# Performance work log

Hardware: AMD Instinct MI355X
Metric: run time of the kernel (lower is better)

## Reference

```python
import jax, jax.numpy as jnp
import numpy as np

GAMMA = 0.99  # init kwarg


def _discounted_returns(ep_rs):
    # reversed running_add = running_add*gamma + r, emitted per step
    def step(carry, r):
        carry = carry * GAMMA + r
        return carry, carry
    _, out = jax.lax.scan(step, jnp.float32(0.0), ep_rs, reverse=True)
    return out  # [T]


def setup_inputs() -> dict:
    key = jax.random.key(0)
    k1, k2, k3 = jax.random.split(key, 3)
    T, A = 2097152, 18
    weight = jax.random.normal(k1, (T, A), dtype=jnp.float32)
    ep_rs = jax.random.normal(k2, (T,), dtype=jnp.float32)
    ep_as = jax.random.randint(k3, (T,), 0, A, dtype=jnp.int64)
    return {"weight": weight, "ep_rs": ep_rs, "ep_as": ep_as}


def reference(weight, ep_rs, ep_as):
    d = _discounted_returns(ep_rs)
    d = d - jnp.mean(d)
    # cross_entropy with reduction='none': -log_softmax(weight)[t, ep_as[t]]
    logp = jax.nn.log_softmax(weight, axis=-1)  # [T, A]
    neg_log_prob = -jnp.take_along_axis(logp, ep_as[:, None], axis=-1)[:, 0]  # [T]
    return jnp.mean(neg_log_prob * d)
```

## Files before the change

### kernel.cpp

```cpp
#include <hip/hip_runtime.h>
#include <math.h>

#define T_TOTAL 2097152
#define A_DIM   18
#define GAMMA_D 0.99

#define CHUNK 256
#define NC    (T_TOTAL / CHUNK)
#define KTR   14
#define CPB   2
#define NB    (NC / CPB)
#define BLK   256
#define WIN   (CPB + KTR - 1)

constexpr double Gp1   = GAMMA_D;
constexpr double Gp2   = Gp1 * Gp1;
constexpr double Gp4   = Gp2 * Gp2;
constexpr double Gp8   = Gp4 * Gp4;
constexpr double Gp16  = Gp8 * Gp8;
constexpr double Gp32  = Gp16 * Gp16;
constexpr double Gp64  = Gp32 * Gp32;
constexpr double Gp128 = Gp64 * Gp64;
constexpr double Gp256 = Gp128 * Gp128;
constexpr double IG    = 1.0 / GAMMA_D;

__global__ __launch_bounds__(BLK, 6)
void k_mega(const float* __restrict__ wgt, const int* __restrict__ act,
            const float* __restrict__ r, double* __restrict__ partials) {
    __shared__ double ldsL[WIN];
    __shared__ double ldsD[CPB * CHUNK];
    __shared__ double red[12];
    const int tid  = threadIdx.x;
    const int lane = tid & 63, wv = tid >> 6;
    const int c0   = blockIdx.x * CPB;
    const double g = GAMMA_D;
    double w4 = 1.0;
    w4 *= (lane & 1)  ? Gp4   : 1.0;
    w4 *= (lane & 2)  ? Gp8   : 1.0;
    w4 *= (lane & 4)  ? Gp16  : 1.0;
    w4 *= (lane & 8)  ? Gp32  : 1.0;
    w4 *= (lane & 16) ? Gp64  : 1.0;
    w4 *= (lane & 32) ? Gp128 : 1.0;

    float4 rwin[4];
    #pragma unroll
    for (int i = 0; i < 4; ++i) {
        const int k  = wv + 4 * i;
        const int cc = c0 + 1 + k;
        rwin[i] = (k < WIN && cc < NC)
                  ? ((const float4*)r)[(size_t)cc * 64 + lane]
                  : make_float4(0, 0, 0, 0);
    }
    const float4 rown = (wv < CPB)
                        ? ((const float4*)r)[(size_t)(c0 + wv) * 64 + lane]
                        : make_float4(0, 0, 0, 0);

    #pragma unroll
    for (int i = 0; i < 4; ++i) {
        const int k = wv + 4 * i;
        if (k < WIN) {
            double val = w4 * ((double)rwin[i].x + g * ((double)rwin[i].y +
                         g * ((double)rwin[i].z + g * (double)rwin[i].w)));
            #pragma unroll
            for (int off = 32; off > 0; off >>= 1) val += __shfl_down(val, off, 64);
            if (lane == 0) ldsL[k] = val;
        }
    }
    __syncthreads();

    if (wv < CPB) {
        double acc_c = 0.0, wG = 1.0;
        #pragma unroll
        for (int m = 0; m < KTR; ++m) { acc_c += wG * ldsL[wv + m]; wG *= Gp256; }
        const double u3 = (double)rown.w;
        const double u2 = (double)rown.z + g * u3;
        const double u1 = (double)rown.y + g * u2;
        const double u0 = (double)rown.x + g * u1;
        double S = w4 * u0;
        #pragma unroll
        for (int off = 1; off < 64; off <<= 1) {
            const double t = __shfl_down(S, off, 64);
            S += (lane + off < 64) ? t : 0.0;
        }
        double Snext = __shfl_down(S, 1, 64);
        if (lane == 63) Snext = 0.0;
        const double A = (1.0 / w4) * (Snext + Gp256 * acc_c);
        double* dp = ldsD + wv * CHUNK + 4 * lane;
        dp[0] = u0 + A;
        dp[1] = u1 + IG * A;
        dp[2] = u2 + (IG * IG) * A;
        dp[3] = u3 + (IG * IG * IG) * A;
    }
    __syncthreads();

    const size_t t0 = (size_t)blockIdx.x * (CPB * CHUNK) + 2 * (size_t)tid;
    float w[36];
    float4* aw = (float4*)w;
    const float4* wp = (const float4*)(wgt + t0 * A_DIM);
    #pragma unroll
    for (int q = 0; q < 9; ++q) aw[q] = wp[q];
    const int2    aa = *(const int2*)(act + t0);
    const double2 dd = *(const double2*)(ldsD + 2 * tid);

    double s_n = 0.0, s_nd = 0.0;
    double s_d = dd.x + dd.y;
    {
        float mx = w[0];
        #pragma unroll
        for (int j = 1; j < A_DIM; ++j) mx = fmaxf(mx, w[j]);
        float s = 0.0f, wsel = 0.0f;
        #pragma unroll
        for (int j = 0; j < A_DIM; ++j) { s += __expf(w[j] - mx); wsel = (j == aa.x) ? w[j] : wsel; }
        const float nlp = mx + __logf(s) - wsel;
        s_n += (double)nlp;  s_nd += (double)nlp * dd.x;
    }
    {
        float mx = w[18];
        #pragma unroll
        for (int j = 1; j < A_DIM; ++j) mx = fmaxf(mx, w[18 + j]);
        float s = 0.0f, wsel = 0.0f;
        #pragma unroll
        for (int j = 0; j < A_DIM; ++j) { s += __expf(w[18 + j] - mx); wsel = (j == aa.y) ? w[18 + j] : wsel; }
        const float nlp = mx + __logf(s) - wsel;
        s_n += (double)nlp;  s_nd += (double)nlp * dd.y;
    }

    #pragma unroll
    for (int off = 32; off > 0; off >>= 1) {
        s_d  += __shfl_down(s_d,  off, 64);
        s_n  += __shfl_down(s_n,  off, 64);
        s_nd += __shfl_down(s_nd, off, 64);
    }
    if (lane == 0) { red[wv*3+0] = s_d; red[wv*3+1] = s_n; red[wv*3+2] = s_nd; }
    __syncthreads();
    if (tid == 0) {
        double pa = 0.0, pb = 0.0, pc = 0.0;
        #pragma unroll
        for (int q = 0; q < 4; ++q) { pa += red[q*3]; pb += red[q*3+1]; pc += red[q*3+2]; }
        partials[blockIdx.x*3+0] = pa;
        partials[blockIdx.x*3+1] = pb;
        partials[blockIdx.x*3+2] = pc;
    }
}

__global__ void k_final(const double* __restrict__ partials, float* __restrict__ out) {
    __shared__ double red[12];
    const int tid = threadIdx.x;
    double a = 0.0, b = 0.0, c = 0.0;
    for (int i = tid; i < NB; i += 256) {
        a += partials[i*3+0];
        b += partials[i*3+1];
        c += partials[i*3+2];
    }
    #pragma unroll
    for (int off = 32; off > 0; off >>= 1) {
        a += __shfl_down(a, off, 64);
        b += __shfl_down(b, off, 64);
        c += __shfl_down(c, off, 64);
    }
    const int lane = tid & 63, wv = tid >> 6;
    if (lane == 0) { red[wv*3+0] = a; red[wv*3+1] = b; red[wv*3+2] = c; }
    __syncthreads();
    if (tid == 0) {
        double A_ = 0.0, B_ = 0.0, C_ = 0.0;
        #pragma unroll
        for (int i = 0; i < 4; ++i) { A_ += red[i*3]; B_ += red[i*3+1]; C_ += red[i*3+2]; }
        const double invT = 1.0 / (double)T_TOTAL;
        out[0] = (float)((C_ - (A_ * invT) * B_) * invT);
    }
}

extern "C" void kernel_launch(void* const* d_in, const int* in_sizes, int n_in,
                              void* d_out, int out_size, void* d_ws, size_t ws_size,
                              hipStream_t stream) {
    const float* weight = (const float*)d_in[0];
    const float* ep_rs  = (const float*)d_in[1];
    const int*   ep_as  = (const int*)  d_in[2];
    float* out = (float*)d_out;

    double* partials = (double*)d_ws;

    k_mega  <<<NB, BLK, 0, stream>>>(weight, ep_as, ep_rs, partials);
    k_final <<<1,  256, 0, stream>>>(partials, out);
}
```

Before: 236.6 us.

## Process eight chunks per block with double-buffered weight loads

Each block now covers eight 256-step chunks instead of two. This shrinks the redundant lookahead window of discounted-return loads relative to the useful work and cuts the number of blocks and partials. The softmax phase loops four times over 512-step tiles, loading the next tile's weights into a second register buffer while the current one is computed. That adds register pressure, so the occupancy hint drops from 6 to 4 blocks per CU, and the grid shrinks to 1024 blocks.

Result: no change. 236.3 us (-0.1%).

```diff
diff --git a/kernel.cpp b/kernel.cpp
--- a/kernel.cpp
+++ b/kernel.cpp
@@ -8,10 +8,11 @@
 #define CHUNK 256
 #define NC    (T_TOTAL / CHUNK)
 #define KTR   14
-#define CPB   2
+#define CPB   8
 #define NB    (NC / CPB)
 #define BLK   256
 #define WIN   (CPB + KTR - 1)
+#define ITERS (CPB * CHUNK / (BLK * 2))
 
 constexpr double Gp1   = GAMMA_D;
 constexpr double Gp2   = Gp1 * Gp1;
@@ -24,7 +25,7 @@
 constexpr double Gp256 = Gp128 * Gp128;
 constexpr double IG    = 1.0 / GAMMA_D;
 
-__global__ __launch_bounds__(BLK, 6)
+__global__ __launch_bounds__(BLK, 4)
 void k_mega(const float* __restrict__ wgt, const int* __restrict__ act,
             const float* __restrict__ r, double* __restrict__ partials) {
     __shared__ double ldsL[WIN];
@@ -42,21 +43,22 @@
     w4 *= (lane & 16) ? Gp64  : 1.0;
     w4 *= (lane & 32) ? Gp128 : 1.0;
 
-    float4 rwin[4];
-    #pragma unroll
-    for (int i = 0; i < 4; ++i) {
+    float4 rwin[6];
+    #pragma unroll
+    for (int i = 0; i < 6; ++i) {
         const int k  = wv + 4 * i;
         const int cc = c0 + 1 + k;
         rwin[i] = (k < WIN && cc < NC)
                   ? ((const float4*)r)[(size_t)cc * 64 + lane]
                   : make_float4(0, 0, 0, 0);
     }
-    const float4 rown = (wv < CPB)
-                        ? ((const float4*)r)[(size_t)(c0 + wv) * 64 + lane]
-                        : make_float4(0, 0, 0, 0);
-
-    #pragma unroll
-    for (int i = 0; i < 4; ++i) {
+    float4 rown[2];
+    #pragma unroll
+    for (int jj = 0; jj < 2; ++jj)
+        rown[jj] = ((const float4*)r)[(size_t)(c0 + wv + 4 * jj) * 64 + lane];
+
+    #pragma unroll
+    for (int i = 0; i < 6; ++i) {
         const int k = wv + 4 * i;
         if (k < WIN) {
             double val = w4 * ((double)rwin[i].x + g * ((double)rwin[i].y +
@@ -68,14 +70,17 @@
     }
     __syncthreads();
 
-    if (wv < CPB) {
+    #pragma unroll
+    for (int jj = 0; jj < 2; ++jj) {
+        const int j = wv + 4 * jj;
         double acc_c = 0.0, wG = 1.0;
         #pragma unroll
-        for (int m = 0; m < KTR; ++m) { acc_c += wG * ldsL[wv + m]; wG *= Gp256; }
-        const double u3 = (double)rown.w;
-        const double u2 = (double)rown.z + g * u3;
-        const double u1 = (double)rown.y + g * u2;
-        const double u0 = (double)rown.x + g * u1;
+        for (int m = 0; m < KTR; ++m) { acc_c += wG * ldsL[j + m]; wG *= Gp256; }
+        const float4 v = rown[jj];
+        const double u3 = (double)v.w;
+        const double u2 = (double)v.z + g * u3;
+        const double u1 = (double)v.y + g * u2;
+        const double u0 = (double)v.x + g * u1;
         double S = w4 * u0;
         #pragma unroll
         for (int off = 1; off < 64; off <<= 1) {
@@ -85,7 +90,7 @@
         double Snext = __shfl_down(S, 1, 64);
         if (lane == 63) Snext = 0.0;
         const double A = (1.0 / w4) * (Snext + Gp256 * acc_c);
-        double* dp = ldsD + wv * CHUNK + 4 * lane;
+        double* dp = ldsD + j * CHUNK + 4 * lane;
         dp[0] = u0 + A;
         dp[1] = u1 + IG * A;
         dp[2] = u2 + (IG * IG) * A;
@@ -93,37 +98,49 @@
     }
     __syncthreads();
 
-    const size_t t0 = (size_t)blockIdx.x * (CPB * CHUNK) + 2 * (size_t)tid;
-    float w[36];
-    float4* aw = (float4*)w;
-    const float4* wp = (const float4*)(wgt + t0 * A_DIM);
-    #pragma unroll
-    for (int q = 0; q < 9; ++q) aw[q] = wp[q];
-    const int2    aa = *(const int2*)(act + t0);
-    const double2 dd = *(const double2*)(ldsD + 2 * tid);
-
-    double s_n = 0.0, s_nd = 0.0;
-    double s_d = dd.x + dd.y;
-    {
-        float mx = w[0];
-        #pragma unroll
-        for (int j = 1; j < A_DIM; ++j) mx = fmaxf(mx, w[j]);
-        float s = 0.0f, wsel = 0.0f;
-        #pragma unroll
-        for (int j = 0; j < A_DIM; ++j) { s += __expf(w[j] - mx); wsel = (j == aa.x) ? w[j] : wsel; }
-        const float nlp = mx + __logf(s) - wsel;
-        s_n += (double)nlp;  s_nd += (double)nlp * dd.x;
-    }
-    {
-        float mx = w[18];
-        #pragma unroll
-        for (int j = 1; j < A_DIM; ++j) mx = fmaxf(mx, w[18 + j]);
-        float s = 0.0f, wsel = 0.0f;
-        #pragma unroll
-        for (int j = 0; j < A_DIM; ++j) { s += __expf(w[18 + j] - mx); wsel = (j == aa.y) ? w[18 + j] : wsel; }
-        const float nlp = mx + __logf(s) - wsel;
-        s_n += (double)nlp;  s_nd += (double)nlp * dd.y;
-    }
+    const size_t base = (size_t)c0 * CHUNK;
+    double s_d = 0.0, s_n = 0.0, s_nd = 0.0;
+
+    auto loadw = [&](float (&wb)[36], int2& aab, int it) {
+        const size_t t0 = base + (size_t)it * 512 + 2 * (size_t)tid;
+        const float4* wp = (const float4*)(wgt + t0 * A_DIM);
+        float4* dst = (float4*)wb;
+        #pragma unroll
+        for (int q = 0; q < 9; ++q) dst[q] = wp[q];
+        aab = *(const int2*)(act + t0);
+    };
+    auto lse2 = [&](const float (&wb)[36], const int2& aab, int it) {
+        const double2 dd = *(const double2*)(ldsD + it * 512 + 2 * tid);
+        s_d += dd.x + dd.y;
+        {
+            float mx = wb[0];
+            #pragma unroll
+            for (int j = 1; j < A_DIM; ++j) mx = fmaxf(mx, wb[j]);
+            float s = 0.0f, wsel = 0.0f;
+            #pragma unroll
+            for (int j = 0; j < A_DIM; ++j) { s += __expf(wb[j] - mx); wsel = (j == aab.x) ? wb[j] : wsel; }
+            const float nlp = mx + __logf(s) - wsel;
+            s_n += (double)nlp;  s_nd += (double)nlp * dd.x;
+        }
+        {
+            float mx = wb[18];
+            #pragma unroll
+            for (int j = 1; j < A_DIM; ++j) mx = fmaxf(mx, wb[18 + j]);
+            float s = 0.0f, wsel = 0.0f;
+            #pragma unroll
+            for (int j = 0; j < A_DIM; ++j) { s += __expf(wb[18 + j] - mx); wsel = (j == aab.y) ? wb[18 + j] : wsel; }
+            const float nlp = mx + __logf(s) - wsel;
+            s_n += (double)nlp;  s_nd += (double)nlp * dd.y;
+        }
+    };
+
+    float wA[36], wB[36];
+    int2 aaA, aaB;
+    loadw(wA, aaA, 0);
+    loadw(wB, aaB, 1);  lse2(wA, aaA, 0);
+    loadw(wA, aaA, 2);  lse2(wB, aaB, 1);
+    loadw(wB, aaB, 3);  lse2(wA, aaA, 2);
+    lse2(wB, aaB, 3);
 
     #pragma unroll
     for (int off = 32; off > 0; off >>= 1) {
```
